# Performance work log

Measured on AMD Instinct MI355X. Metric: run time of the kernel, lower is better.

Reference implementation:

```python
import jax, jax.numpy as jnp
import numpy as np

HID = 1024

def setup_inputs() -> dict:
    key = jax.random.key(0)
    k1, k2, k3, k4, k5 = jax.random.split(key, 5)
    B, S, H = 16, 2048, HID
    queries = jax.random.normal(k1, (B, H), dtype=jnp.float32)
    keys = jax.random.normal(k2, (B, S, H), dtype=jnp.float32)
    values = jax.random.normal(k3, (B, S, H), dtype=jnp.float32)
    # additive_attention params: Linear(2H->H), ReLU, Linear(H->1)
    s1 = 1.0 / np.sqrt(2 * H)
    s2 = 1.0 / np.sqrt(H)
    W1 = jax.random.uniform(k4, (2 * H, H), dtype=jnp.float32, minval=-s1, maxval=s1)
    b1 = jnp.zeros((H,), dtype=jnp.float32)
    W2 = jax.random.uniform(k5, (H, 1), dtype=jnp.float32, minval=-s2, maxval=s2)
    b2 = jnp.zeros((1,), dtype=jnp.float32)
    return {"queries": queries, "keys": keys, "values": values,
            "W1": W1, "b1": b1, "W2": W2, "b2": b2}

def reference(queries, keys, values, W1, b1, W2, b2):
    B, S, H = keys.shape
    # concat expanded query with keys along feature dim: [B,S,2H]
    q_exp = jnp.broadcast_to(queries[:, None, :], (B, S, H))
    concat = jnp.concatenate([q_exp, keys], axis=-1)
    h = jax.nn.relu(jnp.einsum('bsf,fh->bsh', concat, W1) + b1)
    scores = jnp.einsum('bsh,ho->bso', h, W2) + b2          # [B,S,1]
    alphas = jax.nn.softmax(scores, axis=1)                  # softmax over seq
    # context = alphas^T @ values : [B,1,H]
    context = jnp.einsum('bso,bsh->boh', alphas, values)
    return (context, alphas)
```

## Files before the change

kernel.cpp:

```cpp
#include <hip/hip_runtime.h>

#define HID 1024
#define SEQ 2048
#define NB  16

typedef __attribute__((ext_vector_type(8))) short bf16x8;
typedef __attribute__((ext_vector_type(4))) float f32x4;

static __device__ __forceinline__ short f2bf(float f) {
    union { float f; unsigned u; } v; v.f = f;
    unsigned u = v.u + 0x7fffu + ((v.u >> 16) & 1u);
    return (short)(u >> 16);
}
static __device__ __forceinline__ unsigned pk2(float a, float b) {
    return (unsigned)(unsigned short)f2bf(a) | ((unsigned)(unsigned short)f2bf(b) << 16);
}
static __device__ __forceinline__ void glds16(const void* g, void* l) {
    __builtin_amdgcn_global_load_lds(
        (const __attribute__((address_space(1))) unsigned*)g,
        (__attribute__((address_space(3))) unsigned*)l, 16, 0, 0);
}

__global__ __launch_bounds__(256) void prep_all(const float* __restrict__ W1,
                                                const float* __restrict__ queries,
                                                const float* __restrict__ b1,
                                                short* __restrict__ w1t,
                                                float* __restrict__ qproj) {
    __shared__ float shmem[2048];
    const int tid = threadIdx.x;
    int bw = blockIdx.x;

    if (bw < 32) {
        const int f0 = (bw >> 2) * 128;
        const int n0 = (bw & 3) * 256;
#pragma unroll
        for (int j = 0; j < 8; ++j) {
            const int idx = tid * 8 + j;
            const int b = idx >> 7, f = idx & 127;
            shmem[idx] = queries[b * HID + f0 + f];
        }
        __syncthreads();
        float acc[16];
        const float bv = (bw >> 2 == 0) ? b1[n0 + tid] : 0.0f;
#pragma unroll
        for (int b = 0; b < 16; ++b) acc[b] = bv;
        for (int f = 0; f < 128; ++f) {
            const float w = W1[(size_t)(f0 + f) * HID + n0 + tid];
#pragma unroll
            for (int b = 0; b < 16; ++b)
                acc[b] += shmem[b * 128 + f] * w;
        }
#pragma unroll
        for (int b = 0; b < 16; ++b)
            atomicAdd(&qproj[b * HID + n0 + tid], acc[b]);
        return;
    }
    bw -= 32;
    {
        float (*t)[33] = (float(*)[33])shmem;
        const int k0 = (bw & 31) * 32;
        const int n0 = (bw >> 5) * 32;
        const int tx = tid & 31, ty = tid >> 5;
#pragma unroll
        for (int i = 0; i < 32; i += 8)
            t[ty + i][tx] = W1[(size_t)(HID + k0 + ty + i) * HID + n0 + tx];
        __syncthreads();
#pragma unroll
        for (int i = 0; i < 32; i += 8)
            w1t[(size_t)(n0 + ty + i) * HID + k0 + tx] = f2bf(t[tx][ty + i]);
    }
}

__global__ __launch_bounds__(256) void score_gemm(const float* __restrict__ keys,
                                                  const short* __restrict__ w1t,
                                                  const float* __restrict__ qproj,
                                                  const float* __restrict__ W2,
                                                  float* __restrict__ scores) {
    __shared__ short As[128 * 32];
    __shared__ short Bs[128 * 32];

    const int tid  = threadIdx.x;
    const int lane = tid & 63;
    const int wave = tid >> 6;
    const int id   = blockIdx.x;
    const int n_blk = (id >> 3) & 7;
    const int m_blk = (id >> 6) * 8 + (id & 7);
    const int n0 = n_blk * 128;
    const int m0 = m_blk * 128;
    const int batch = m0 >> 11;
    const int wm = wave >> 1, wn = wave & 1;
    const int q = lane >> 4, c = lane & 15;
    const int xr = c & 3;

    const int lrow = lane >> 2;
    const int lk   = ((lane & 3) ^ (lrow & 3)) << 3;

    const int ar  = tid >> 1;
    const int ah  = (tid & 1) * 16;
    const int as0 = (((ah >> 3) + 0) ^ (ar & 3)) << 3;
    const int as1 = (((ah >> 3) + 1) ^ (ar & 3)) << 3;
    const float* asrc = keys + (size_t)(m0 + ar) * HID + ah;

    f32x4 acc[4][4] = {};

    for (int k0 = 0; k0 < HID; k0 += 32) {
#pragma unroll
        for (int call = 0; call < 2; ++call) {
            const int rbase = (wave * 2 + call) * 16;
            glds16(w1t + (size_t)(n0 + rbase + lrow) * HID + k0 + lk,
                   &Bs[rbase * 32]);
        }
        {
            const float4 v0 = *(const float4*)(asrc + k0 + 0);
            const float4 v1 = *(const float4*)(asrc + k0 + 4);
            const float4 v2 = *(const float4*)(asrc + k0 + 8);
            const float4 v3 = *(const float4*)(asrc + k0 + 12);
            int4 o0, o1;
            o0.x = (int)pk2(v0.x, v0.y); o0.y = (int)pk2(v0.z, v0.w);
            o0.z = (int)pk2(v1.x, v1.y); o0.w = (int)pk2(v1.z, v1.w);
            o1.x = (int)pk2(v2.x, v2.y); o1.y = (int)pk2(v2.z, v2.w);
            o1.z = (int)pk2(v3.x, v3.y); o1.w = (int)pk2(v3.z, v3.w);
            *(int4*)&As[ar * 32 + as0] = o0;
            *(int4*)&As[ar * 32 + as1] = o1;
        }
        __syncthreads();

        bf16x8 af[4], bf[4];
#pragma unroll
        for (int i = 0; i < 4; ++i)
            af[i] = *(const bf16x8*)&As[(wm * 64 + i * 16 + c) * 32 + ((q ^ xr) << 3)];
#pragma unroll
        for (int i = 0; i < 4; ++i)
            bf[i] = *(const bf16x8*)&Bs[(wn * 64 + i * 16 + c) * 32 + ((q ^ xr) << 3)];
#pragma unroll
        for (int mi = 0; mi < 4; ++mi)
#pragma unroll
            for (int ni = 0; ni < 4; ++ni)
                acc[mi][ni] = __builtin_amdgcn_mfma_f32_16x16x32_bf16(af[mi], bf[ni], acc[mi][ni], 0, 0, 0);
        __syncthreads();
    }

    const float* qp = qproj + batch * HID + n0 + wn * 64;
    const float* w2 = W2 + n0 + wn * 64;
    float psum[4][4] = {};
#pragma unroll
    for (int ni = 0; ni < 4; ++ni) {
        const float qv = qp[ni * 16 + c];
        const float wv = w2[ni * 16 + c];
#pragma unroll
        for (int mi = 0; mi < 4; ++mi)
#pragma unroll
            for (int r = 0; r < 4; ++r)
                psum[mi][r] += fmaxf(acc[mi][ni][r] + qv, 0.f) * wv;
    }
#pragma unroll
    for (int m = 1; m < 16; m <<= 1)
#pragma unroll
        for (int mi = 0; mi < 4; ++mi)
#pragma unroll
            for (int r = 0; r < 4; ++r)
                psum[mi][r] += __shfl_xor(psum[mi][r], m, 64);
    if (c == 0) {
#pragma unroll
        for (int mi = 0; mi < 4; ++mi) {
            const int row = m0 + wm * 64 + mi * 16 + q * 4;
#pragma unroll
            for (int r = 0; r < 4; ++r)
                atomicAdd(&scores[row + r], psum[mi][r]);
        }
    }
}

__global__ __launch_bounds__(256) void softmax_k(const float* __restrict__ scores,
                                                 float* __restrict__ alphas,
                                                 float* __restrict__ ctx) {
    __shared__ float red[256];
    const int b = blockIdx.x;
    const int tid = threadIdx.x;
    float4 z = {0.f, 0.f, 0.f, 0.f};
    *(float4*)(ctx + b * HID + tid * 4) = z;

    float loc[8];
    float mx = -1e30f;
#pragma unroll
    for (int i = 0; i < 8; ++i) {
        loc[i] = scores[b * SEQ + tid + i * 256];
        mx = fmaxf(mx, loc[i]);
    }
    red[tid] = mx; __syncthreads();
    for (int s = 128; s > 0; s >>= 1) {
        if (tid < s) red[tid] = fmaxf(red[tid], red[tid + s]);
        __syncthreads();
    }
    mx = red[0]; __syncthreads();
    float sum = 0.f;
#pragma unroll
    for (int i = 0; i < 8; ++i) { loc[i] = expf(loc[i] - mx); sum += loc[i]; }
    red[tid] = sum; __syncthreads();
    for (int s = 128; s > 0; s >>= 1) {
        if (tid < s) red[tid] += red[tid + s];
        __syncthreads();
    }
    const float inv = 1.0f / red[0];
#pragma unroll
    for (int i = 0; i < 8; ++i) alphas[b * SEQ + tid + i * 256] = loc[i] * inv;
}

__global__ __launch_bounds__(256) void context_k(const float* __restrict__ alphas,
                                                 const float* __restrict__ values,
                                                 float* __restrict__ context) {
    __shared__ float al[64];
    const int b = blockIdx.y;
    const int s0 = blockIdx.x * 64;
    const int tid = threadIdx.x;
    if (tid < 64) al[tid] = alphas[b * SEQ + s0 + tid];
    __syncthreads();
    const int col = tid * 4;
    float4 acc = {0.f, 0.f, 0.f, 0.f};
#pragma unroll 4
    for (int i = 0; i < 64; ++i) {
        const float a = al[i];
        const float4 v = *(const float4*)(values + (size_t)(b * SEQ + s0 + i) * HID + col);
        acc.x += a * v.x; acc.y += a * v.y; acc.z += a * v.z; acc.w += a * v.w;
    }
    float* cp = context + b * HID + col;
    atomicAdd(cp + 0, acc.x);
    atomicAdd(cp + 1, acc.y);
    atomicAdd(cp + 2, acc.z);
    atomicAdd(cp + 3, acc.w);
}

extern "C" void kernel_launch(void* const* d_in, const int* in_sizes, int n_in,
                              void* d_out, int out_size, void* d_ws, size_t ws_size,
                              hipStream_t stream) {
    const float* queries = (const float*)d_in[0];
    const float* keys    = (const float*)d_in[1];
    const float* values  = (const float*)d_in[2];
    const float* W1      = (const float*)d_in[3];
    const float* b1      = (const float*)d_in[4];
    const float* W2      = (const float*)d_in[5];

    float* out_ctx   = (float*)d_out;
    float* out_alpha = (float*)d_out + NB * HID;

    char* ws = (char*)d_ws;
    float* scores = (float*)ws;
    float* qproj  = (float*)(ws + 131072);
    short* w1t    = (short*)(ws + 196608);

    hipMemsetAsync(ws, 0, 196608, stream);

    prep_all<<<32 + 1024, 256, 0, stream>>>(W1, queries, b1, w1t, qproj);

    score_gemm<<<2048, 256, 0, stream>>>(keys, w1t, qproj, W2, scores);

    softmax_k<<<NB, 256, 0, stream>>>(scores, out_alpha, out_ctx);
    context_k<<<dim3(32, NB), 256, 0, stream>>>(out_alpha, values, out_ctx);
}
```

Measured before the change: 431.3 us.

## Double-buffer score GEMM tiles, use hardware bf16 pack, widen context grid

The score GEMM now keeps two LDS buffers for the A and B tiles. It prefetches the next keys tile into registers and issues the W1 global-to-LDS loads one iteration ahead, so memory latency overlaps the MFMA work. The fp32→bf16 conversion switches from software rounding to the v_cvt_pk_bf16_f32 instruction, the LDS swizzle pattern changes, and occupancy is hinted at 4 blocks per CU. The context kernel is split into twice as many blocks of 32 rows, which adds parallelism at the cost of more atomics.

```diff
diff --git a/kernel.cpp b/kernel.cpp
--- a/kernel.cpp
+++ b/kernel.cpp
@@ -12,8 +12,10 @@
     unsigned u = v.u + 0x7fffu + ((v.u >> 16) & 1u);
     return (short)(u >> 16);
 }
-static __device__ __forceinline__ unsigned pk2(float a, float b) {
-    return (unsigned)(unsigned short)f2bf(a) | ((unsigned)(unsigned short)f2bf(b) << 16);
+static __device__ __forceinline__ unsigned pk2h(float a, float b) {
+    unsigned r;
+    asm("v_cvt_pk_bf16_f32 %0, %1, %2" : "=v"(r) : "v"(a), "v"(b));
+    return r;
 }
 static __device__ __forceinline__ void glds16(const void* g, void* l) {
     __builtin_amdgcn_global_load_lds(
@@ -71,13 +73,13 @@
     }
 }
 
-__global__ __launch_bounds__(256) void score_gemm(const float* __restrict__ keys,
-                                                  const short* __restrict__ w1t,
-                                                  const float* __restrict__ qproj,
-                                                  const float* __restrict__ W2,
-                                                  float* __restrict__ scores) {
-    __shared__ short As[128 * 32];
-    __shared__ short Bs[128 * 32];
+__global__ __launch_bounds__(256, 4) void score_gemm(const float* __restrict__ keys,
+                                                     const short* __restrict__ w1t,
+                                                     const float* __restrict__ qproj,
+                                                     const float* __restrict__ W2,
+                                                     float* __restrict__ scores) {
+    __shared__ short As[2][128 * 32];
+    __shared__ short Bs[2][128 * 32];
 
     const int tid  = threadIdx.x;
     const int lane = tid & 63;
@@ -90,48 +92,76 @@
     const int batch = m0 >> 11;
     const int wm = wave >> 1, wn = wave & 1;
     const int q = lane >> 4, c = lane & 15;
-    const int xr = c & 3;
+    const int xr = (c >> 1) & 3;
 
     const int lrow = lane >> 2;
-    const int lk   = ((lane & 3) ^ (lrow & 3)) << 3;
+    const int lk   = ((lane & 3) ^ ((lane >> 3) & 3)) << 3;
+    const short* bsrc = w1t + (size_t)(n0 + lrow) * HID + lk;
 
     const int ar  = tid >> 1;
     const int ah  = (tid & 1) * 16;
-    const int as0 = (((ah >> 3) + 0) ^ (ar & 3)) << 3;
-    const int as1 = (((ah >> 3) + 1) ^ (ar & 3)) << 3;
+    const int g_ar = (ar >> 1) & 3;
+    const int as0 = (((ah >> 3) + 0) ^ g_ar) << 3;
+    const int as1 = (((ah >> 3) + 1) ^ g_ar) << 3;
     const float* asrc = keys + (size_t)(m0 + ar) * HID + ah;
 
     f32x4 acc[4][4] = {};
 
-    for (int k0 = 0; k0 < HID; k0 += 32) {
-#pragma unroll
-        for (int call = 0; call < 2; ++call) {
-            const int rbase = (wave * 2 + call) * 16;
-            glds16(w1t + (size_t)(n0 + rbase + lrow) * HID + k0 + lk,
-                   &Bs[rbase * 32]);
-        }
-        {
-            const float4 v0 = *(const float4*)(asrc + k0 + 0);
-            const float4 v1 = *(const float4*)(asrc + k0 + 4);
-            const float4 v2 = *(const float4*)(asrc + k0 + 8);
-            const float4 v3 = *(const float4*)(asrc + k0 + 12);
+    float4 ua0 = *(const float4*)(asrc + 0);
+    float4 ua1 = *(const float4*)(asrc + 4);
+    float4 ua2 = *(const float4*)(asrc + 8);
+    float4 ua3 = *(const float4*)(asrc + 12);
+#pragma unroll
+    for (int call = 0; call < 2; ++call) {
+        const int rbase = (wave * 2 + call) * 16;
+        glds16(bsrc + (size_t)rbase * HID, &Bs[0][rbase * 32]);
+    }
+    {
+        int4 o0, o1;
+        o0.x = (int)pk2h(ua0.x, ua0.y); o0.y = (int)pk2h(ua0.z, ua0.w);
+        o0.z = (int)pk2h(ua1.x, ua1.y); o0.w = (int)pk2h(ua1.z, ua1.w);
+        o1.x = (int)pk2h(ua2.x, ua2.y); o1.y = (int)pk2h(ua2.z, ua2.w);
+        o1.z = (int)pk2h(ua3.x, ua3.y); o1.w = (int)pk2h(ua3.z, ua3.w);
+        *(int4*)&As[0][ar * 32 + as0] = o0;
+        *(int4*)&As[0][ar * 32 + as1] = o1;
+    }
+    ua0 = *(const float4*)(asrc + 32);
+    ua1 = *(const float4*)(asrc + 36);
+    ua2 = *(const float4*)(asrc + 40);
+    ua3 = *(const float4*)(asrc + 44);
+    __syncthreads();
+
+    for (int t = 0; t < 32; ++t) {
+        const int cur = t & 1, nxt = cur ^ 1;
+        if (t < 31) {
+            const int k1 = (t + 1) * 32;
+#pragma unroll
+            for (int call = 0; call < 2; ++call) {
+                const int rbase = (wave * 2 + call) * 16;
+                glds16(bsrc + (size_t)rbase * HID + k1, &Bs[nxt][rbase * 32]);
+            }
             int4 o0, o1;
-            o0.x = (int)pk2(v0.x, v0.y); o0.y = (int)pk2(v0.z, v0.w);
-            o0.z = (int)pk2(v1.x, v1.y); o0.w = (int)pk2(v1.z, v1.w);
-            o1.x = (int)pk2(v2.x, v2.y); o1.y = (int)pk2(v2.z, v2.w);
-            o1.z = (int)pk2(v3.x, v3.y); o1.w = (int)pk2(v3.z, v3.w);
-            *(int4*)&As[ar * 32 + as0] = o0;
-            *(int4*)&As[ar * 32 + as1] = o1;
-        }
-        __syncthreads();
-
+            o0.x = (int)pk2h(ua0.x, ua0.y); o0.y = (int)pk2h(ua0.z, ua0.w);
+            o0.z = (int)pk2h(ua1.x, ua1.y); o0.w = (int)pk2h(ua1.z, ua1.w);
+            o1.x = (int)pk2h(ua2.x, ua2.y); o1.y = (int)pk2h(ua2.z, ua2.w);
+            o1.z = (int)pk2h(ua3.x, ua3.y); o1.w = (int)pk2h(ua3.z, ua3.w);
+            *(int4*)&As[nxt][ar * 32 + as0] = o0;
+            *(int4*)&As[nxt][ar * 32 + as1] = o1;
+            if (t < 30) {
+                const float* s2 = asrc + (t + 2) * 32;
+                ua0 = *(const float4*)(s2 + 0);
+                ua1 = *(const float4*)(s2 + 4);
+                ua2 = *(const float4*)(s2 + 8);
+                ua3 = *(const float4*)(s2 + 12);
+            }
+        }
         bf16x8 af[4], bf[4];
 #pragma unroll
         for (int i = 0; i < 4; ++i)
-            af[i] = *(const bf16x8*)&As[(wm * 64 + i * 16 + c) * 32 + ((q ^ xr) << 3)];
+            af[i] = *(const bf16x8*)&As[cur][(wm * 64 + i * 16 + c) * 32 + ((q ^ xr) << 3)];
 #pragma unroll
         for (int i = 0; i < 4; ++i)
-            bf[i] = *(const bf16x8*)&Bs[(wn * 64 + i * 16 + c) * 32 + ((q ^ xr) << 3)];
+            bf[i] = *(const bf16x8*)&Bs[cur][(wn * 64 + i * 16 + c) * 32 + ((q ^ xr) << 3)];
 #pragma unroll
         for (int mi = 0; mi < 4; ++mi)
 #pragma unroll
@@ -209,16 +239,16 @@
 __global__ __launch_bounds__(256) void context_k(const float* __restrict__ alphas,
                                                  const float* __restrict__ values,
                                                  float* __restrict__ context) {
-    __shared__ float al[64];
+    __shared__ float al[32];
     const int b = blockIdx.y;
-    const int s0 = blockIdx.x * 64;
+    const int s0 = blockIdx.x * 32;
     const int tid = threadIdx.x;
-    if (tid < 64) al[tid] = alphas[b * SEQ + s0 + tid];
+    if (tid < 32) al[tid] = alphas[b * SEQ + s0 + tid];
     __syncthreads();
     const int col = tid * 4;
     float4 acc = {0.f, 0.f, 0.f, 0.f};
-#pragma unroll 4
-    for (int i = 0; i < 64; ++i) {
+#pragma unroll 8
+    for (int i = 0; i < 32; ++i) {
         const float a = al[i];
         const float4 v = *(const float4*)(values + (size_t)(b * SEQ + s0 + i) * HID + col);
         acc.x += a * v.x; acc.y += a * v.y; acc.z += a * v.z; acc.w += a * v.w;
@@ -248,12 +278,12 @@
     float* qproj  = (float*)(ws + 131072);
     short* w1t    = (short*)(ws + 196608);
 
-    hipMemsetAsync(ws, 0, 196608, stream);
+    (void)hipMemsetAsync(ws, 0, 196608, stream);
 
     prep_all<<<32 + 1024, 256, 0, stream>>>(W1, queries, b1, w1t, qproj);
 
     score_gemm<<<2048, 256, 0, stream>>>(keys, w1t, qproj, W2, scores);
 
     softmax_k<<<NB, 256, 0, stream>>>(scores, out_alpha, out_ctx);
-    context_k<<<dim3(32, NB), 256, 0, stream>>>(out_alpha, values, out_ctx);
-}
+    context_k<<<dim3(64, NB), 256, 0, stream>>>(out_alpha, values, out_ctx);
+}
```

Measured after the change: 411.6 us. 4.6% less time.

## Pre-convert keys to bf16, replace atomics with partial buffers, use hardware bf16 packing

Applied to the files above, without the earlier changes.

Adds a pre-pass in prep_all that converts all keys to bf16 in the workspace, so the score GEMM can load A tiles straight into LDS with global_load_lds instead of loading fp32 and converting in registers. All atomicAdd reductions (qproj, scores, context) become deterministic partial buffers that later kernels sum, which also removes the memset. A hardware v_cvt_pk_bf16_f32 instruction replaces the software rounding, the LDS swizzle is changed and launch bounds are raised. The cost is an extra full read and write of keys in bf16 plus an extra reduce kernel, and the fast path only runs when the workspace is large enough.

```diff
diff --git a/kernel.cpp b/kernel.cpp
--- a/kernel.cpp
+++ b/kernel.cpp
@@ -12,8 +12,10 @@
     unsigned u = v.u + 0x7fffu + ((v.u >> 16) & 1u);
     return (short)(u >> 16);
 }
-static __device__ __forceinline__ unsigned pk2(float a, float b) {
-    return (unsigned)(unsigned short)f2bf(a) | ((unsigned)(unsigned short)f2bf(b) << 16);
+static __device__ __forceinline__ unsigned pk2h(float a, float b) {
+    unsigned r;
+    asm("v_cvt_pk_bf16_f32 %0, %1, %2" : "=v"(r) : "v"(a), "v"(b));
+    return r;
 }
 static __device__ __forceinline__ void glds16(const void* g, void* l) {
     __builtin_amdgcn_global_load_lds(
@@ -24,15 +26,18 @@
 __global__ __launch_bounds__(256) void prep_all(const float* __restrict__ W1,
                                                 const float* __restrict__ queries,
                                                 const float* __restrict__ b1,
+                                                const float* __restrict__ keys,
                                                 short* __restrict__ w1t,
-                                                float* __restrict__ qproj) {
+                                                float* __restrict__ qproj_part,
+                                                short* __restrict__ kbf,
+                                                int nconv) {
     __shared__ float shmem[2048];
     const int tid = threadIdx.x;
     int bw = blockIdx.x;
 
     if (bw < 32) {
-        const int f0 = (bw >> 2) * 128;
-        const int n0 = (bw & 3) * 256;
+        const int fc = bw >> 2, nc = bw & 3;
+        const int f0 = fc * 128, n0 = nc * 256;
 #pragma unroll
         for (int j = 0; j < 8; ++j) {
             const int idx = tid * 8 + j;
@@ -41,7 +46,7 @@
         }
         __syncthreads();
         float acc[16];
-        const float bv = (bw >> 2 == 0) ? b1[n0 + tid] : 0.0f;
+        const float bv = (fc == 0) ? b1[n0 + tid] : 0.0f;
 #pragma unroll
         for (int b = 0; b < 16; ++b) acc[b] = bv;
         for (int f = 0; f < 128; ++f) {
@@ -52,11 +57,11 @@
         }
 #pragma unroll
         for (int b = 0; b < 16; ++b)
-            atomicAdd(&qproj[b * HID + n0 + tid], acc[b]);
+            qproj_part[(size_t)(fc * 16 + b) * HID + n0 + tid] = acc[b];
         return;
     }
     bw -= 32;
-    {
+    if (bw < 1024) {
         float (*t)[33] = (float(*)[33])shmem;
         const int k0 = (bw & 31) * 32;
         const int n0 = (bw >> 5) * 32;
@@ -68,16 +73,30 @@
 #pragma unroll
         for (int i = 0; i < 32; i += 8)
             w1t[(size_t)(n0 + ty + i) * HID + k0 + tx] = f2bf(t[tx][ty + i]);
-    }
-}
-
-__global__ __launch_bounds__(256) void score_gemm(const float* __restrict__ keys,
-                                                  const short* __restrict__ w1t,
-                                                  const float* __restrict__ qproj,
-                                                  const float* __restrict__ W2,
-                                                  float* __restrict__ scores) {
+        return;
+    }
+    bw -= 1024;
+    if (bw < nconv) {
+        const size_t i = ((size_t)bw * 256 + tid) * 8;
+        const float4 a = *(const float4*)(keys + i);
+        const float4 b = *(const float4*)(keys + i + 4);
+        int4 o;
+        o.x = (int)pk2h(a.x, a.y); o.y = (int)pk2h(a.z, a.w);
+        o.z = (int)pk2h(b.x, b.y); o.w = (int)pk2h(b.z, b.w);
+        *(int4*)(kbf + i) = o;
+    }
+}
+
+template<int PRE>
+__global__ __launch_bounds__(256, 4) void score_gemm(const float* __restrict__ keys,
+                                                     const short* __restrict__ kbf,
+                                                     const short* __restrict__ w1t,
+                                                     const float* __restrict__ qproj_part,
+                                                     const float* __restrict__ W2,
+                                                     float* __restrict__ scores_part) {
     __shared__ short As[128 * 32];
     __shared__ short Bs[128 * 32];
+    __shared__ float red[4][64];
 
     const int tid  = threadIdx.x;
     const int lane = tid & 63;
@@ -90,16 +109,19 @@
     const int batch = m0 >> 11;
     const int wm = wave >> 1, wn = wave & 1;
     const int q = lane >> 4, c = lane & 15;
-    const int xr = c & 3;
+    const int xr = (c >> 1) & 3;
 
     const int lrow = lane >> 2;
-    const int lk   = ((lane & 3) ^ (lrow & 3)) << 3;
+    const int lk   = ((lane & 3) ^ ((lane >> 3) & 3)) << 3;
+    const short* bsrc = w1t + (size_t)(n0 + lrow) * HID + lk;
+    const short* asrc = kbf + (size_t)(m0 + lrow) * HID + lk;
 
     const int ar  = tid >> 1;
     const int ah  = (tid & 1) * 16;
-    const int as0 = (((ah >> 3) + 0) ^ (ar & 3)) << 3;
-    const int as1 = (((ah >> 3) + 1) ^ (ar & 3)) << 3;
-    const float* asrc = keys + (size_t)(m0 + ar) * HID + ah;
+    const int g_ar = (ar >> 1) & 3;
+    const int as0 = (((ah >> 3) + 0) ^ g_ar) << 3;
+    const int as1 = (((ah >> 3) + 1) ^ g_ar) << 3;
+    const float* afsrc = keys + (size_t)(m0 + ar) * HID + ah;
 
     f32x4 acc[4][4] = {};
 
@@ -107,19 +129,24 @@
 #pragma unroll
         for (int call = 0; call < 2; ++call) {
             const int rbase = (wave * 2 + call) * 16;
-            glds16(w1t + (size_t)(n0 + rbase + lrow) * HID + k0 + lk,
-                   &Bs[rbase * 32]);
+            glds16(bsrc + (size_t)rbase * HID + k0, &Bs[rbase * 32]);
         }
-        {
-            const float4 v0 = *(const float4*)(asrc + k0 + 0);
-            const float4 v1 = *(const float4*)(asrc + k0 + 4);
-            const float4 v2 = *(const float4*)(asrc + k0 + 8);
-            const float4 v3 = *(const float4*)(asrc + k0 + 12);
+        if (PRE) {
+#pragma unroll
+            for (int call = 0; call < 2; ++call) {
+                const int rbase = (wave * 2 + call) * 16;
+                glds16(asrc + (size_t)rbase * HID + k0, &As[rbase * 32]);
+            }
+        } else {
+            const float4 v0 = *(const float4*)(afsrc + k0 + 0);
+            const float4 v1 = *(const float4*)(afsrc + k0 + 4);
+            const float4 v2 = *(const float4*)(afsrc + k0 + 8);
+            const float4 v3 = *(const float4*)(afsrc + k0 + 12);
             int4 o0, o1;
-            o0.x = (int)pk2(v0.x, v0.y); o0.y = (int)pk2(v0.z, v0.w);
-            o0.z = (int)pk2(v1.x, v1.y); o0.w = (int)pk2(v1.z, v1.w);
-            o1.x = (int)pk2(v2.x, v2.y); o1.y = (int)pk2(v2.z, v2.w);
-            o1.z = (int)pk2(v3.x, v3.y); o1.w = (int)pk2(v3.z, v3.w);
+            o0.x = (int)pk2h(v0.x, v0.y); o0.y = (int)pk2h(v0.z, v0.w);
+            o0.z = (int)pk2h(v1.x, v1.y); o0.w = (int)pk2h(v1.z, v1.w);
+            o1.x = (int)pk2h(v2.x, v2.y); o1.y = (int)pk2h(v2.z, v2.w);
+            o1.z = (int)pk2h(v3.x, v3.y); o1.w = (int)pk2h(v3.z, v3.w);
             *(int4*)&As[ar * 32 + as0] = o0;
             *(int4*)&As[ar * 32 + as1] = o1;
         }
@@ -140,12 +167,15 @@
         __syncthreads();
     }
 
-    const float* qp = qproj + batch * HID + n0 + wn * 64;
     const float* w2 = W2 + n0 + wn * 64;
     float psum[4][4] = {};
 #pragma unroll
     for (int ni = 0; ni < 4; ++ni) {
-        const float qv = qp[ni * 16 + c];
+        const int n = n0 + wn * 64 + ni * 16 + c;
+        float qv = 0.f;
+#pragma unroll
+        for (int p = 0; p < 8; ++p)
+            qv += qproj_part[(size_t)(p * 16 + batch) * HID + n];
         const float wv = w2[ni * 16 + c];
 #pragma unroll
         for (int mi = 0; mi < 4; ++mi)
@@ -162,30 +192,37 @@
                 psum[mi][r] += __shfl_xor(psum[mi][r], m, 64);
     if (c == 0) {
 #pragma unroll
-        for (int mi = 0; mi < 4; ++mi) {
-            const int row = m0 + wm * 64 + mi * 16 + q * 4;
+        for (int mi = 0; mi < 4; ++mi)
 #pragma unroll
             for (int r = 0; r < 4; ++r)
-                atomicAdd(&scores[row + r], psum[mi][r]);
-        }
-    }
-}
-
-__global__ __launch_bounds__(256) void softmax_k(const float* __restrict__ scores,
-                                                 float* __restrict__ alphas,
-                                                 float* __restrict__ ctx) {
+                red[wave][mi * 16 + q * 4 + r] = psum[mi][r];
+    }
+    __syncthreads();
+    if (tid < 128) {
+        const int wm2 = tid >> 6, idx = tid & 63;
+        scores_part[(size_t)n_blk * (SEQ * NB) + m0 + wm2 * 64 + idx] =
+            red[wm2 * 2][idx] + red[wm2 * 2 + 1][idx];
+    }
+}
+
+__global__ __launch_bounds__(256) void softmax_k(const float* __restrict__ scores_part,
+                                                 float* __restrict__ alphas) {
     __shared__ float red[256];
     const int b = blockIdx.x;
     const int tid = threadIdx.x;
-    float4 z = {0.f, 0.f, 0.f, 0.f};
-    *(float4*)(ctx + b * HID + tid * 4) = z;
+    const float* sp = scores_part + b * SEQ;
 
     float loc[8];
     float mx = -1e30f;
 #pragma unroll
     for (int i = 0; i < 8; ++i) {
-        loc[i] = scores[b * SEQ + tid + i * 256];
-        mx = fmaxf(mx, loc[i]);
+        const int s = tid + i * 256;
+        float v = 0.f;
+#pragma unroll
+        for (int p = 0; p < 8; ++p)
+            v += sp[(size_t)p * (SEQ * NB) + s];
+        loc[i] = v;
+        mx = fmaxf(mx, v);
     }
     red[tid] = mx; __syncthreads();
     for (int s = 128; s > 0; s >>= 1) {
@@ -206,28 +243,38 @@
     for (int i = 0; i < 8; ++i) alphas[b * SEQ + tid + i * 256] = loc[i] * inv;
 }
 
-__global__ __launch_bounds__(256) void context_k(const float* __restrict__ alphas,
-                                                 const float* __restrict__ values,
-                                                 float* __restrict__ context) {
+__global__ __launch_bounds__(256) void context_part_k(const float* __restrict__ alphas,
+                                                      const float* __restrict__ values,
+                                                      float* __restrict__ ctx_part) {
     __shared__ float al[64];
     const int b = blockIdx.y;
-    const int s0 = blockIdx.x * 64;
+    const int sb = blockIdx.x;
+    const int s0 = sb * 64;
     const int tid = threadIdx.x;
     if (tid < 64) al[tid] = alphas[b * SEQ + s0 + tid];
     __syncthreads();
     const int col = tid * 4;
     float4 acc = {0.f, 0.f, 0.f, 0.f};
-#pragma unroll 4
+#pragma unroll 8
     for (int i = 0; i < 64; ++i) {
         const float a = al[i];
         const float4 v = *(const float4*)(values + (size_t)(b * SEQ + s0 + i) * HID + col);
         acc.x += a * v.x; acc.y += a * v.y; acc.z += a * v.z; acc.w += a * v.w;
     }
-    float* cp = context + b * HID + col;
-    atomicAdd(cp + 0, acc.x);
-    atomicAdd(cp + 1, acc.y);
-    atomicAdd(cp + 2, acc.z);
-    atomicAdd(cp + 3, acc.w);
+    *(float4*)(ctx_part + (size_t)(sb * NB + b) * HID + col) = acc;
+}
+
+__global__ __launch_bounds__(256) void ctx_reduce_k(const float* __restrict__ ctx_part,
+                                                    float* __restrict__ context) {
+    const int b = blockIdx.x;
+    const int col = threadIdx.x * 4;
+    float4 s = {0.f, 0.f, 0.f, 0.f};
+#pragma unroll
+    for (int p = 0; p < 32; ++p) {
+        const float4 v = *(const float4*)(ctx_part + (size_t)(p * NB + b) * HID + col);
+        s.x += v.x; s.y += v.y; s.z += v.z; s.w += v.w;
+    }
+    *(float4*)(context + b * HID + col) = s;
 }
 
 extern "C" void kernel_launch(void* const* d_in, const int* in_sizes, int n_in,
@@ -244,16 +291,24 @@
     float* out_alpha = (float*)d_out + NB * HID;
 
     char* ws = (char*)d_ws;
-    float* scores = (float*)ws;
-    float* qproj  = (float*)(ws + 131072);
-    short* w1t    = (short*)(ws + 196608);
-
-    hipMemsetAsync(ws, 0, 196608, stream);
-
-    prep_all<<<32 + 1024, 256, 0, stream>>>(W1, queries, b1, w1t, qproj);
-
-    score_gemm<<<2048, 256, 0, stream>>>(keys, w1t, qproj, W2, scores);
-
-    softmax_k<<<NB, 256, 0, stream>>>(scores, out_alpha, out_ctx);
-    context_k<<<dim3(32, NB), 256, 0, stream>>>(out_alpha, values, out_ctx);
-}
+    float* scores_part = (float*)ws;
+    float* qproj_part  = (float*)(ws + 1048576);
+    float* ctx_part    = (float*)(ws + 1572864);
+    short* w1t         = (short*)(ws + 3670016);
+    short* kbf         = (short*)(ws + 5767168);
+
+    const bool pre = ws_size >= 72876032ull;
+    const int nconv = pre ? 16384 : 0;
+
+    prep_all<<<32 + 1024 + nconv, 256, 0, stream>>>(
+        W1, queries, b1, keys, w1t, qproj_part, kbf, nconv);
+
+    if (pre)
+        score_gemm<1><<<2048, 256, 0, stream>>>(keys, kbf, w1t, qproj_part, W2, scores_part);
+    else
+        score_gemm<0><<<2048, 256, 0, stream>>>(keys, kbf, w1t, qproj_part, W2, scores_part);
+
+    softmax_k<<<NB, 256, 0, stream>>>(scores_part, out_alpha);
+    context_part_k<<<dim3(32, NB), 256, 0, stream>>>(out_alpha, values, ctx_part);
+    ctx_reduce_k<<<NB, 256, 0, stream>>>(ctx_part, out_ctx);
+}
```

After: 372.7 us. 1.16x faster.
